# Kernel tuning notes

Measured on AMD Instinct MI355X. Metric: run time of the kernel, lower is better.

Reference implementation:

```python
import jax, jax.numpy as jnp
import numpy as np

N = 50000      # nodes
E = 1_600_000  # edges (avg degree 32)
G = 2000       # graphs in batch
H = 2          # attention heads
C = 64         # out_channels
IN = 64        # in_channels
NEG_SLOPE = 0.2


def setup_inputs() -> dict:
    key = jax.random.key(0)
    ks = jax.random.split(key, 6)
    x = jax.random.normal(ks[0], (N, IN), dtype=jnp.float32)
    edge_index = jax.random.randint(ks[1], (2, E), 0, N, dtype=jnp.int32)
    batch = jnp.sort(jax.random.randint(ks[2], (N,), 0, G, dtype=jnp.int32))
    # GATConv params: lin weight [H*C, IN] (glorot-ish), att vectors, bias [C]
    W = jax.random.normal(ks[3], (H * C, IN), dtype=jnp.float32) * (1.0 / np.sqrt(IN))
    att_src = jax.random.normal(ks[4], (1, H, C), dtype=jnp.float32) * 0.1
    att_dst = jax.random.normal(ks[5], (1, H, C), dtype=jnp.float32) * 0.1
    bias = jnp.zeros((C,), dtype=jnp.float32)
    return {"x": x, "edge_index": edge_index, "batch": batch,
            "W": W, "att_src": att_src, "att_dst": att_dst, "bias": bias}


def reference(x, edge_index, batch, W, att_src, att_dst, bias):
    # --- GATConv (PyG semantics: add_self_loops=True, concat=False -> head mean + bias) ---
    loops = jnp.arange(N, dtype=edge_index.dtype)
    src = jnp.concatenate([edge_index[0], loops])  # [E+N]
    dst = jnp.concatenate([edge_index[1], loops])  # [E+N]

    xp = (x @ W.T).reshape(N, H, C)                 # projected node feats [N,H,C]
    a_src = jnp.sum(xp * att_src, axis=-1)          # [N,H]
    a_dst = jnp.sum(xp * att_dst, axis=-1)          # [N,H]

    e = jax.nn.leaky_relu(a_src[src] + a_dst[dst], NEG_SLOPE)  # [E+N,H]
    # segment softmax over incoming edges of each destination node
    m = jax.ops.segment_max(e, dst, num_segments=N)            # [N,H]
    e = jnp.exp(e - m[dst])
    s = jax.ops.segment_sum(e, dst, num_segments=N)            # [N,H]
    alpha = e / s[dst]                                         # [E+N,H]

    msg = xp[src] * alpha[:, :, None]                          # [E+N,H,C]
    out = jax.ops.segment_sum(msg, dst, num_segments=N)        # [N,H,C]
    h_nodes = out.mean(axis=1) + bias                          # [N,C]

    # --- global_mean_pool ---
    sums = jax.ops.segment_sum(h_nodes, batch, num_segments=G)                     # [G,C]
    cnt = jax.ops.segment_sum(jnp.ones((N, 1), h_nodes.dtype), batch, num_segments=G)
    h_graphs = sums / jnp.maximum(cnt, 1.0)                                        # [G,C]
    return (h_nodes, h_graphs)
```

## Files before the change

### kernel.cpp

```cpp
#include <hip/hip_runtime.h>
#include <hip/hip_bf16.h>

#define H 2
#define C 64
#define IN_CH 64
#define HC (H*C)
#define NEG_SLOPE 0.2f
#define NBUCK_MAX 256
#define NBLK 1024

__global__ __launch_bounds__(128) void proj_kernel(
    const float* __restrict__ x, const float* __restrict__ W,
    const float* __restrict__ att_src, const float* __restrict__ att_dst,
    __hip_bfloat16* __restrict__ xp, float* __restrict__ asrc,
    float* __restrict__ adst, int N) {
    int t = threadIdx.x;
    float w[64];
    const float4* wr = reinterpret_cast<const float4*>(W + (size_t)t * IN_CH);
#pragma unroll
    for (int q = 0; q < 16; q++) {
        float4 v = wr[q];
        w[4 * q] = v.x; w[4 * q + 1] = v.y; w[4 * q + 2] = v.z; w[4 * q + 3] = v.w;
    }
    float a_s = att_src[t], a_d = att_dst[t];
    int lane = t & 63, head = t >> 6;
    for (int n = blockIdx.x; n < N; n += gridDim.x) {
        const float* xr = x + (size_t)n * IN_CH;
        float acc = 0.f;
#pragma unroll
        for (int k = 0; k < 64; k++) acc = fmaf(w[k], xr[k], acc);
        xp[(size_t)n * HC + t] = __float2bfloat16(acc);
        float as = acc * a_s, ad = acc * a_d;
#pragma unroll
        for (int d = 32; d > 0; d >>= 1) {
            as += __shfl_xor(as, d, 64);
            ad += __shfl_xor(ad, d, 64);
        }
        if (lane == 0) {
            asrc[(size_t)n * H + head] = as;
            adst[(size_t)n * H + head] = ad;
        }
    }
}

__global__ __launch_bounds__(256) void hist_kernel(const int* __restrict__ dstE,
                                                   int* __restrict__ hist,
                                                   int E, int nbuck, int chunkE) {
    __shared__ int lh[NBUCK_MAX];
    for (int t = threadIdx.x; t < nbuck; t += 256) lh[t] = 0;
    __syncthreads();
    int beg = blockIdx.x * chunkE;
    int end = min(beg + chunkE, E);
    for (int i = beg + threadIdx.x; i < end; i += 256)
        atomicAdd(&lh[dstE[i] >> 8], 1);
    __syncthreads();
    for (int t = threadIdx.x; t < nbuck; t += 256)
        hist[t * NBLK + blockIdx.x] = lh[t];
}

__global__ __launch_bounds__(256) void scan_rows_kernel(int* __restrict__ hist,
                                                        int* __restrict__ rowsum) {
    int b = blockIdx.x, t = threadIdx.x;
    int* row = hist + b * NBLK;
    int v[4];
    int s = 0;
#pragma unroll
    for (int j = 0; j < 4; j++) { v[j] = row[t * 4 + j]; s += v[j]; }
    __shared__ int sh[256];
    sh[t] = s;
    __syncthreads();
    for (int d = 1; d < 256; d <<= 1) {
        int u = (t >= d) ? sh[t - d] : 0;
        __syncthreads();
        sh[t] += u;
        __syncthreads();
    }
    int run = sh[t] - s;
#pragma unroll
    for (int j = 0; j < 4; j++) { row[t * 4 + j] = run; run += v[j]; }
    if (t == 255) rowsum[b] = sh[255];
}

__device__ __forceinline__ void base_scan(const int* rowsum, int nbuck,
                                          int* bse, int* rs, int t) {
    int v = (t < nbuck) ? rowsum[t] : 0;
    if (t < 256) { bse[t] = v; rs[t] = v; }
    __syncthreads();
    for (int d = 1; d < 256; d <<= 1) {
        int u = (t >= d && t < 256) ? bse[t - d] : 0;
        __syncthreads();
        if (t < 256) bse[t] += u;
        __syncthreads();
    }
    if (t < 256) bse[t] -= rs[t];
    __syncthreads();
}

__global__ __launch_bounds__(256) void bucket_scatter_kernel(
    const int* __restrict__ srcE, const int* __restrict__ dstE,
    const int* __restrict__ hist, const int* __restrict__ rowsum,
    int* __restrict__ staged, int E, int nbuck, int chunkE) {
    __shared__ int bse[256], rs[256], cur[NBUCK_MAX];
    int t = threadIdx.x;
    base_scan(rowsum, nbuck, bse, rs, t);
    for (int i = t; i < nbuck; i += 256)
        cur[i] = hist[i * NBLK + blockIdx.x] + bse[i];
    __syncthreads();
    int beg = blockIdx.x * chunkE;
    int end = min(beg + chunkE, E);
    for (int i = beg + t; i < end; i += 256) {
        int s = srcE[i], d = dstE[i];
        int pos = atomicAdd(&cur[d >> 8], 1);
        staged[pos] = s | ((d & 255) << 20);
    }
}

__global__ __launch_bounds__(512) void bucket_csr_kernel(
    const int* __restrict__ staged, const int* __restrict__ rowsum,
    int* __restrict__ off, int* __restrict__ csr, int N, int nbuck, int E) {
    int b = blockIdx.x, t = threadIdx.x;
    __shared__ int bse[256], rs[256], lh[256], sh[256], cur[256];
    base_scan(rowsum, nbuck, bse, rs, t);
    int beg = bse[b], end = beg + rs[b];
    if (t < 256) lh[t] = 0;
    __syncthreads();
    for (int i = beg + t; i < end; i += 512)
        atomicAdd(&lh[staged[i] >> 20], 1);
    __syncthreads();
    int v = (t < 256) ? lh[t] : 0;
    if (t < 256) sh[t] = v;
    __syncthreads();
    for (int d = 1; d < 256; d <<= 1) {
        int u = (t >= d && t < 256) ? sh[t - d] : 0;
        __syncthreads();
        if (t < 256) sh[t] += u;
        __syncthreads();
    }
    if (t < 256) {
        int ex = sh[t] - v;
        int nd = b * 256 + t;
        if (nd < N) off[nd] = beg + ex;
        if (nd == N - 1) off[N] = end;
        cur[t] = beg + ex;
    }
    __syncthreads();
    for (int i = beg + t; i < end; i += 512) {
        int e = staged[i];
        int pos = atomicAdd(&cur[e >> 20], 1);
        csr[pos] = e & 0xFFFFF;
    }
}

template<int NB16>
__device__ __forceinline__ void gather_fma(const uint* __restrict__ xpw,
                                           const int* __restrict__ sidx,
                                           const float2* __restrict__ swt,
                                           int lane, float& accx, float& accy) {
    uint bu[NB16 * 16];
#pragma unroll
    for (int j = 0; j < NB16 * 16; j++) {
        int s2 = sidx[j];
        bu[j] = xpw[(size_t)s2 * 64 + lane];
    }
#pragma unroll
    for (int j = 0; j < NB16 * 16; j++) {
        float2 wv = swt[j];
        float wgt = (lane < 32) ? wv.x : wv.y;
        accx = fmaf(wgt, __uint_as_float(bu[j] << 16), accx);
        accy = fmaf(wgt, __uint_as_float(bu[j] & 0xffff0000u), accy);
    }
}

__global__ __launch_bounds__(256, 4) void aggregate_kernel(
    const __hip_bfloat16* __restrict__ xp, const float2* __restrict__ asrc,
    const float2* __restrict__ adst, const int* __restrict__ off,
    const int* __restrict__ csr, const float* __restrict__ bias,
    float* __restrict__ out, int N) {
    __shared__ int sidx[4][64];
    __shared__ float2 swt[4][64];
    int wid = threadIdx.x >> 6;
    int n = blockIdx.x * 4 + wid;
    if (n >= N) return;
    int lane = threadIdx.x & 63;
    int* si = sidx[wid];
    float2* sw = swt[wid];
    int o0 = off[n];
    int degE = off[n + 1] - o0;
    float2 ad = adst[n];
    float2 asn = asrc[n];
    float es0 = asn.x + ad.x; es0 = (es0 > 0.f) ? es0 : NEG_SLOPE * es0;
    float es1 = asn.y + ad.y; es1 = (es1 > 0.f) ? es1 : NEG_SLOPE * es1;
    float ws0 = __expf(es0), ws1 = __expf(es1);
    float s0 = (lane == 0) ? ws0 : 0.f;
    float s1 = (lane == 0) ? ws1 : 0.f;

    const uint* xpw = reinterpret_cast<const uint*>(xp);
    float accx, accy;
    {
        float wgt = (lane < 32) ? ws0 : ws1;
        uint u = xpw[(size_t)n * 64 + lane];
        accx = wgt * __uint_as_float(u << 16);
        accy = wgt * __uint_as_float(u & 0xffff0000u);
    }

    for (int base = 0; base < degE; base += 64) {
        int i = base + lane;
        int idx = 0;
        float w0 = 0.f, w1 = 0.f;
        if (i < degE) {
            idx = csr[o0 + i];
            float2 as = asrc[idx];
            float t0 = as.x + ad.x; t0 = (t0 > 0.f) ? t0 : NEG_SLOPE * t0;
            float t1 = as.y + ad.y; t1 = (t1 > 0.f) ? t1 : NEG_SLOPE * t1;
            w0 = __expf(t0);
            w1 = __expf(t1);
        }
        s0 += w0;
        s1 += w1;
        si[lane] = idx;
        sw[lane] = make_float2(w0, w1);
        int cnt = min(degE - base, 64);
        int nb16 = (cnt + 15) >> 4;
        switch (nb16) {
            case 1: gather_fma<1>(xpw, si, sw, lane, accx, accy); break;
            case 2: gather_fma<2>(xpw, si, sw, lane, accx, accy); break;
            case 3: gather_fma<3>(xpw, si, sw, lane, accx, accy); break;
            default: gather_fma<4>(xpw, si, sw, lane, accx, accy); break;
        }
    }
#pragma unroll
    for (int d = 32; d > 0; d >>= 1) {
        s0 += __shfl_xor(s0, d, 64);
        s1 += __shfl_xor(s1, d, 64);
    }
    float inv = (lane < 32) ? (1.f / s0) : (1.f / s1);
    accx *= inv;
    accy *= inv;
    float ox = 0.5f * (accx + __shfl_xor(accx, 32, 64));
    float oy = 0.5f * (accy + __shfl_xor(accy, 32, 64));
    if (lane < 32) {
        float vx = ox + bias[2 * lane];
        float vy = oy + bias[2 * lane + 1];
        *reinterpret_cast<float2*>(out + (size_t)n * C + 2 * lane) = make_float2(vx, vy);
    }
}

__global__ __launch_bounds__(64) void pool_kernel(const float* __restrict__ hn,
                                                  const int* __restrict__ batch,
                                                  float* __restrict__ outG, int N, int G) {
    int g = blockIdx.x;
    int c = threadIdx.x;
    int lo = 0, hi = N;
    while (lo < hi) { int mid = (lo + hi) >> 1; if (batch[mid] < g) lo = mid + 1; else hi = mid; }
    int beg = lo;
    lo = beg; hi = N;
    while (lo < hi) { int mid = (lo + hi) >> 1; if (batch[mid] < g + 1) lo = mid + 1; else hi = mid; }
    int end = lo;
    float s = 0.f;
    for (int n = beg; n < end; n++) s += hn[(size_t)n * C + c];
    outG[(size_t)g * C + c] = s / fmaxf((float)(end - beg), 1.f);
}

extern "C" void kernel_launch(void* const* d_in, const int* in_sizes, int n_in,
                              void* d_out, int out_size, void* d_ws, size_t ws_size,
                              hipStream_t stream) {
    const float* x       = (const float*)d_in[0];
    const int*   edge    = (const int*)d_in[1];
    const int*   batch   = (const int*)d_in[2];
    const float* W       = (const float*)d_in[3];
    const float* att_src = (const float*)d_in[4];
    const float* att_dst = (const float*)d_in[5];
    const float* bias    = (const float*)d_in[6];

    int N = in_sizes[0] / IN_CH;
    int E = in_sizes[1] / 2;
    int G = out_size / C - N;
    int nbuck = (N + 255) >> 8;
    int chunkE = (E + NBLK - 1) / NBLK;

    char* p = (char*)d_ws;
    auto alloc = [&](size_t bytes) {
        char* r = p;
        p += (bytes + 255) & ~(size_t)255;
        return r;
    };
    __hip_bfloat16* xp = (__hip_bfloat16*)alloc((size_t)N * HC * 2);
    float* asrc    = (float*)alloc((size_t)N * H * 4);
    float* adst    = (float*)alloc((size_t)N * H * 4);
    int*   hist    = (int*)alloc((size_t)nbuck * NBLK * 4);
    int*   rowsum  = (int*)alloc((size_t)(nbuck + 1) * 4);
    int*   off     = (int*)alloc((size_t)(N + 1) * 4);
    int*   staged  = (int*)alloc((size_t)E * 4);
    int*   csr     = (int*)alloc((size_t)E * 4);

    const int* srcE = edge;
    const int* dstE = edge + E;

    proj_kernel<<<2048, 128, 0, stream>>>(x, W, att_src, att_dst, xp, asrc, adst, N);
    hist_kernel<<<NBLK, 256, 0, stream>>>(dstE, hist, E, nbuck, chunkE);
    scan_rows_kernel<<<nbuck, 256, 0, stream>>>(hist, rowsum);
    bucket_scatter_kernel<<<NBLK, 256, 0, stream>>>(srcE, dstE, hist, rowsum,
                                                    staged, E, nbuck, chunkE);
    bucket_csr_kernel<<<nbuck, 512, 0, stream>>>(staged, rowsum, off, csr, N, nbuck, E);
    aggregate_kernel<<<(N + 3) / 4, 256, 0, stream>>>(xp, (const float2*)asrc, (const float2*)adst,
                                                      off, csr, bias, (float*)d_out, N);
    pool_kernel<<<G, 64, 0, stream>>>((const float*)d_out, batch, (float*)d_out + (size_t)N * C,
                                      N, G);
}
```

Measured before the change: 226.5 us.

## Fuse projection with single-pass atomic bucket scatter; parallelize graph pooling

Replaces the histogram, row-scan and bucket-scatter kernels with one kernel that first computes the projection and attention logits. It then reserves per-bucket slots through global atomic counters, writing edges into fixed-capacity (CAP) bucket regions. The CSR kernel scans the bucket counts itself, and the pool kernel splits each graph's nodes across four warps with a shared-memory reduction. This removes several launches and a full pass over the edges, but CAP assumes no bucket exceeds the fixed capacity, and edge order within buckets becomes nondeterministic.

```diff
diff --git a/kernel.cpp b/kernel.cpp
--- a/kernel.cpp
+++ b/kernel.cpp
@@ -8,124 +8,96 @@
 #define NEG_SLOPE 0.2f
 #define NBUCK_MAX 256
 #define NBLK 1024
-
-__global__ __launch_bounds__(128) void proj_kernel(
-    const float* __restrict__ x, const float* __restrict__ W,
-    const float* __restrict__ att_src, const float* __restrict__ att_dst,
-    __hip_bfloat16* __restrict__ xp, float* __restrict__ asrc,
-    float* __restrict__ adst, int N) {
-    int t = threadIdx.x;
-    float w[64];
-    const float4* wr = reinterpret_cast<const float4*>(W + (size_t)t * IN_CH);
-#pragma unroll
-    for (int q = 0; q < 16; q++) {
-        float4 v = wr[q];
-        w[4 * q] = v.x; w[4 * q + 1] = v.y; w[4 * q + 2] = v.z; w[4 * q + 3] = v.w;
-    }
-    float a_s = att_src[t], a_d = att_dst[t];
-    int lane = t & 63, head = t >> 6;
-    for (int n = blockIdx.x; n < N; n += gridDim.x) {
-        const float* xr = x + (size_t)n * IN_CH;
-        float acc = 0.f;
-#pragma unroll
-        for (int k = 0; k < 64; k++) acc = fmaf(w[k], xr[k], acc);
-        xp[(size_t)n * HC + t] = __float2bfloat16(acc);
-        float as = acc * a_s, ad = acc * a_d;
-#pragma unroll
-        for (int d = 32; d > 0; d >>= 1) {
-            as += __shfl_xor(as, d, 64);
-            ad += __shfl_xor(ad, d, 64);
-        }
-        if (lane == 0) {
-            asrc[(size_t)n * H + head] = as;
-            adst[(size_t)n * H + head] = ad;
-        }
-    }
-}
-
-__global__ __launch_bounds__(256) void hist_kernel(const int* __restrict__ dstE,
-                                                   int* __restrict__ hist,
-                                                   int E, int nbuck, int chunkE) {
-    __shared__ int lh[NBUCK_MAX];
-    for (int t = threadIdx.x; t < nbuck; t += 256) lh[t] = 0;
-    __syncthreads();
-    int beg = blockIdx.x * chunkE;
-    int end = min(beg + chunkE, E);
-    for (int i = beg + threadIdx.x; i < end; i += 256)
+#define CAP 12288
+
+__global__ __launch_bounds__(256) void proj_scatter_kernel(
+    const float* __restrict__ x, const int* __restrict__ edge,
+    const float* __restrict__ W, const float* __restrict__ att_src,
+    const float* __restrict__ att_dst, __hip_bfloat16* __restrict__ xp,
+    float* __restrict__ asrc, float* __restrict__ adst,
+    int* __restrict__ cnt, int* __restrict__ staged, int N, int E) {
+    const int tid = threadIdx.x, bid = blockIdx.x;
+    const int nbuck = (N + 255) >> 8;
+    const int chunkE = (E + NBLK - 1) / NBLK;
+    const int* srcE = edge;
+    const int* dstE = edge + E;
+
+    {
+        int ch = tid & 127, sub = tid >> 7, lane = tid & 63, head = (tid >> 6) & 1;
+        float w[64];
+        const float4* wr = reinterpret_cast<const float4*>(W + (size_t)ch * IN_CH);
+#pragma unroll
+        for (int q = 0; q < 16; q++) {
+            float4 v = wr[q];
+            w[4 * q] = v.x; w[4 * q + 1] = v.y; w[4 * q + 2] = v.z; w[4 * q + 3] = v.w;
+        }
+        float a_s = att_src[ch], a_d = att_dst[ch];
+        for (int n0 = bid * 2; n0 < N; n0 += NBLK * 2) {
+            int n = n0 + sub;
+            if (n < N) {
+                const float* xr = x + (size_t)n * IN_CH;
+                float acc = 0.f;
+#pragma unroll
+                for (int k = 0; k < 64; k++) acc = fmaf(w[k], xr[k], acc);
+                xp[(size_t)n * HC + ch] = __float2bfloat16(acc);
+                float as = acc * a_s, ad = acc * a_d;
+#pragma unroll
+                for (int d = 32; d > 0; d >>= 1) {
+                    as += __shfl_xor(as, d, 64);
+                    ad += __shfl_xor(ad, d, 64);
+                }
+                if (lane == 0) {
+                    asrc[2 * n + head] = as;
+                    adst[2 * n + head] = ad;
+                }
+            }
+        }
+    }
+
+    __shared__ int lh[NBUCK_MAX], bse[NBUCK_MAX], lcur[NBUCK_MAX];
+    for (int i = tid; i < nbuck; i += 256) { lh[i] = 0; lcur[i] = 0; }
+    __syncthreads();
+    int beg = bid * chunkE, end = min(beg + chunkE, E);
+    for (int i = beg + tid; i < end; i += 256)
         atomicAdd(&lh[dstE[i] >> 8], 1);
     __syncthreads();
-    for (int t = threadIdx.x; t < nbuck; t += 256)
-        hist[t * NBLK + blockIdx.x] = lh[t];
-}
-
-__global__ __launch_bounds__(256) void scan_rows_kernel(int* __restrict__ hist,
-                                                        int* __restrict__ rowsum) {
-    int b = blockIdx.x, t = threadIdx.x;
-    int* row = hist + b * NBLK;
-    int v[4];
-    int s = 0;
-#pragma unroll
-    for (int j = 0; j < 4; j++) { v[j] = row[t * 4 + j]; s += v[j]; }
-    __shared__ int sh[256];
-    sh[t] = s;
-    __syncthreads();
-    for (int d = 1; d < 256; d <<= 1) {
-        int u = (t >= d) ? sh[t - d] : 0;
-        __syncthreads();
-        sh[t] += u;
-        __syncthreads();
-    }
-    int run = sh[t] - s;
-#pragma unroll
-    for (int j = 0; j < 4; j++) { row[t * 4 + j] = run; run += v[j]; }
-    if (t == 255) rowsum[b] = sh[255];
-}
-
-__device__ __forceinline__ void base_scan(const int* rowsum, int nbuck,
-                                          int* bse, int* rs, int t) {
-    int v = (t < nbuck) ? rowsum[t] : 0;
-    if (t < 256) { bse[t] = v; rs[t] = v; }
-    __syncthreads();
-    for (int d = 1; d < 256; d <<= 1) {
-        int u = (t >= d && t < 256) ? bse[t - d] : 0;
-        __syncthreads();
-        if (t < 256) bse[t] += u;
-        __syncthreads();
-    }
-    if (t < 256) bse[t] -= rs[t];
-    __syncthreads();
-}
-
-__global__ __launch_bounds__(256) void bucket_scatter_kernel(
-    const int* __restrict__ srcE, const int* __restrict__ dstE,
-    const int* __restrict__ hist, const int* __restrict__ rowsum,
-    int* __restrict__ staged, int E, int nbuck, int chunkE) {
-    __shared__ int bse[256], rs[256], cur[NBUCK_MAX];
-    int t = threadIdx.x;
-    base_scan(rowsum, nbuck, bse, rs, t);
-    for (int i = t; i < nbuck; i += 256)
-        cur[i] = hist[i * NBLK + blockIdx.x] + bse[i];
-    __syncthreads();
-    int beg = blockIdx.x * chunkE;
-    int end = min(beg + chunkE, E);
-    for (int i = beg + t; i < end; i += 256) {
+    for (int i = tid; i < nbuck; i += 256) {
+        int c = lh[i];
+        bse[i] = (c > 0) ? atomicAdd(&cnt[i], c) : 0;
+    }
+    __syncthreads();
+    for (int i = beg + tid; i < end; i += 256) {
         int s = srcE[i], d = dstE[i];
-        int pos = atomicAdd(&cur[d >> 8], 1);
-        staged[pos] = s | ((d & 255) << 20);
+        int b = d >> 8;
+        int l = atomicAdd(&lcur[b], 1);
+        staged[(size_t)b * CAP + bse[b] + l] = s | ((d & 255) << 20);
     }
 }
 
 __global__ __launch_bounds__(512) void bucket_csr_kernel(
-    const int* __restrict__ staged, const int* __restrict__ rowsum,
-    int* __restrict__ off, int* __restrict__ csr, int N, int nbuck, int E) {
+    const int* __restrict__ staged, const int* __restrict__ cnt,
+    int* __restrict__ off, int* __restrict__ csr, int N, int nbuck) {
     int b = blockIdx.x, t = threadIdx.x;
     __shared__ int bse[256], rs[256], lh[256], sh[256], cur[256];
-    base_scan(rowsum, nbuck, bse, rs, t);
-    int beg = bse[b], end = beg + rs[b];
+    {
+        int v = (t < nbuck) ? cnt[t] : 0;
+        if (t < 256) { bse[t] = v; rs[t] = v; }
+        __syncthreads();
+        for (int d = 1; d < 256; d <<= 1) {
+            int u = (t >= d && t < 256) ? bse[t - d] : 0;
+            __syncthreads();
+            if (t < 256) bse[t] += u;
+            __syncthreads();
+        }
+        if (t < 256) bse[t] -= rs[t];
+        __syncthreads();
+    }
+    int base = bse[b], size = rs[b];
+    const int* st = staged + (size_t)b * CAP;
     if (t < 256) lh[t] = 0;
     __syncthreads();
-    for (int i = beg + t; i < end; i += 512)
-        atomicAdd(&lh[staged[i] >> 20], 1);
+    for (int i = t; i < size; i += 512)
+        atomicAdd(&lh[st[i] >> 20], 1);
     __syncthreads();
     int v = (t < 256) ? lh[t] : 0;
     if (t < 256) sh[t] = v;
@@ -139,13 +111,13 @@
     if (t < 256) {
         int ex = sh[t] - v;
         int nd = b * 256 + t;
-        if (nd < N) off[nd] = beg + ex;
-        if (nd == N - 1) off[N] = end;
-        cur[t] = beg + ex;
-    }
-    __syncthreads();
-    for (int i = beg + t; i < end; i += 512) {
-        int e = staged[i];
+        if (nd < N) off[nd] = base + ex;
+        if (nd == N - 1) off[N] = base + size;
+        cur[t] = base + ex;
+    }
+    __syncthreads();
+    for (int i = t; i < size; i += 512) {
+        int e = st[i];
         int pos = atomicAdd(&cur[e >> 20], 1);
         csr[pos] = e & 0xFFFFF;
     }
@@ -219,8 +191,8 @@
         s1 += w1;
         si[lane] = idx;
         sw[lane] = make_float2(w0, w1);
-        int cnt = min(degE - base, 64);
-        int nb16 = (cnt + 15) >> 4;
+        int cnt2 = min(degE - base, 64);
+        int nb16 = (cnt2 + 15) >> 4;
         switch (nb16) {
             case 1: gather_fma<1>(xpw, si, sw, lane, accx, accy); break;
             case 2: gather_fma<2>(xpw, si, sw, lane, accx, accy); break;
@@ -245,20 +217,26 @@
     }
 }
 
-__global__ __launch_bounds__(64) void pool_kernel(const float* __restrict__ hn,
-                                                  const int* __restrict__ batch,
-                                                  float* __restrict__ outG, int N, int G) {
+__global__ __launch_bounds__(256) void pool_kernel(const float* __restrict__ hn,
+                                                   const int* __restrict__ batch,
+                                                   float* __restrict__ outG, int N, int G) {
     int g = blockIdx.x;
-    int c = threadIdx.x;
+    int c = threadIdx.x & 63, r = threadIdx.x >> 6;
     int lo = 0, hi = N;
     while (lo < hi) { int mid = (lo + hi) >> 1; if (batch[mid] < g) lo = mid + 1; else hi = mid; }
     int beg = lo;
-    lo = beg; hi = N;
-    while (lo < hi) { int mid = (lo + hi) >> 1; if (batch[mid] < g + 1) lo = mid + 1; else hi = mid; }
+    hi = N;
+    while (lo < hi) { int mid = (lo + hi) >> 1; if (batch[mid] <= g) lo = mid + 1; else hi = mid; }
     int end = lo;
     float s = 0.f;
-    for (int n = beg; n < end; n++) s += hn[(size_t)n * C + c];
-    outG[(size_t)g * C + c] = s / fmaxf((float)(end - beg), 1.f);
+    for (int n = beg + r; n < end; n += 4) s += hn[(size_t)n * C + c];
+    __shared__ float red[256];
+    red[threadIdx.x] = s;
+    __syncthreads();
+    if (r == 0) {
+        float tot = red[c] + red[64 + c] + red[128 + c] + red[192 + c];
+        outG[(size_t)g * C + c] = tot / fmaxf((float)(end - beg), 1.f);
+    }
 }
 
 extern "C" void kernel_launch(void* const* d_in, const int* in_sizes, int n_in,
@@ -276,7 +254,6 @@
     int E = in_sizes[1] / 2;
     int G = out_size / C - N;
     int nbuck = (N + 255) >> 8;
-    int chunkE = (E + NBLK - 1) / NBLK;
 
     char* p = (char*)d_ws;
     auto alloc = [&](size_t bytes) {
@@ -287,23 +264,19 @@
     __hip_bfloat16* xp = (__hip_bfloat16*)alloc((size_t)N * HC * 2);
     float* asrc    = (float*)alloc((size_t)N * H * 4);
     float* adst    = (float*)alloc((size_t)N * H * 4);
-    int*   hist    = (int*)alloc((size_t)nbuck * NBLK * 4);
-    int*   rowsum  = (int*)alloc((size_t)(nbuck + 1) * 4);
+    int*   cnt     = (int*)alloc((size_t)nbuck * 4);
     int*   off     = (int*)alloc((size_t)(N + 1) * 4);
-    int*   staged  = (int*)alloc((size_t)E * 4);
+    int*   staged  = (int*)alloc((size_t)nbuck * CAP * 4);
     int*   csr     = (int*)alloc((size_t)E * 4);
 
-    const int* srcE = edge;
-    const int* dstE = edge + E;
-
-    proj_kernel<<<2048, 128, 0, stream>>>(x, W, att_src, att_dst, xp, asrc, adst, N);
-    hist_kernel<<<NBLK, 256, 0, stream>>>(dstE, hist, E, nbuck, chunkE);
-    scan_rows_kernel<<<nbuck, 256, 0, stream>>>(hist, rowsum);
-    bucket_scatter_kernel<<<NBLK, 256, 0, stream>>>(srcE, dstE, hist, rowsum,
-                                                    staged, E, nbuck, chunkE);
-    bucket_csr_kernel<<<nbuck, 512, 0, stream>>>(staged, rowsum, off, csr, N, nbuck, E);
-    aggregate_kernel<<<(N + 3) / 4, 256, 0, stream>>>(xp, (const float2*)asrc, (const float2*)adst,
-                                                      off, csr, bias, (float*)d_out, N);
-    pool_kernel<<<G, 64, 0, stream>>>((const float*)d_out, batch, (float*)d_out + (size_t)N * C,
-                                      N, G);
-}
+    hipMemsetAsync(cnt, 0, (size_t)nbuck * 4, stream);
+
+    proj_scatter_kernel<<<NBLK, 256, 0, stream>>>(x, edge, W, att_src, att_dst,
+                                                  xp, asrc, adst, cnt, staged, N, E);
+    bucket_csr_kernel<<<nbuck, 512, 0, stream>>>(staged, cnt, off, csr, N, nbuck);
+    aggregate_kernel<<<(N + 3) / 4, 256, 0, stream>>>(xp, (const float2*)asrc,
+                                                      (const float2*)adst, off, csr, bias,
+                                                      (float*)d_out, N);
+    pool_kernel<<<G, 256, 0, stream>>>((const float*)d_out, batch,
+                                       (float*)d_out + (size_t)N * C, N, G);
+}
```

Measured after the change: 246.2 us. +8.7%, slower.
